# Performance work log

Hardware: AMD Instinct MI355X
Metric: run time of the kernel (lower is better)

The kernel has to match this reference:

```python
import jax, jax.numpy as jnp
import numpy as np

B = 128           # graphs per batch (cell.num_graphs)
N0 = 706          # genes per graph
NF = 3            # num_feature
DIM = 64          # dim_cell
LAYERS = 3        # layer_cell
VIEW_E = [2268, 6872, 3088, 3150]   # per-graph edges per view (from forward slices)
EPS = 1e-5


def _make_clusters():
    ns = [N0]
    cs = []
    for _ in range(LAYERS):
        c = np.arange(ns[-1]) // 2
        cs.append(c)
        ns.append(int(c.max()) + 1)
    return cs, ns

CLUSTERS, NS = _make_clusters()      # NS = [706, 353, 177, 89]
FINAL = NS[-1]                        # final_node


def _pool_edges(e, c):
    # PyG max_pool pool_edge: relabel by cluster, drop self-loops, coalesce
    s, d = c[e[0]], c[e[1]]
    m = s != d
    return np.unique(np.stack([s[m], d[m]]), axis=1)


def _with_self_loops(e, n):
    sl = np.arange(n, dtype=e.dtype)
    return np.concatenate([e, np.stack([sl, sl])], axis=1)


def _batch(e, n):
    off = (np.arange(B, dtype=e.dtype) * n)
    return (e[:, None, :] + off[None, :, None]).reshape(2, -1)


def setup_inputs():
    rng = np.random.default_rng(0)
    key = jax.random.key(0)
    ks = jax.random.split(key, 32)
    inp = {}
    for j, ne in enumerate(VIEW_E):
        src = rng.integers(0, N0, ne)
        dst = (src + 1 + rng.integers(0, N0 - 1, ne)) % N0
        raw = np.stack([src, dst]).astype(np.int64)
        for i in range(LAYERS):
            gat_e = _batch(_with_self_loops(raw, NS[i]), NS[i])
            inp[f"edges_v{j}_l{i}"] = jnp.asarray(gat_e, jnp.int32)
            raw = _pool_edges(raw, CLUSTERS[i])
    for i in range(LAYERS):
        cb = (CLUSTERS[i][None, :] + (np.arange(B) * NS[i + 1])[:, None]).reshape(-1)
        inp[f"cluster_l{i}"] = jnp.asarray(cb, jnp.int32)

    def nrm(k, shape, scale):
        return jax.random.normal(k, shape, jnp.float32) * scale

    inp["x"] = nrm(ks[0], (B * N0, NF), 1.0)
    dims = [NF, DIM, DIM]
    t = 1
    for i in range(LAYERS):
        inp[f"W{i}"] = nrm(ks[t], (dims[i], DIM), dims[i] ** -0.5); t += 1
        inp[f"asrc{i}"] = nrm(ks[t], (DIM,), 0.1); t += 1
        inp[f"adst{i}"] = nrm(ks[t], (DIM,), 0.1); t += 1
        inp[f"b{i}"] = jnp.zeros((DIM,), jnp.float32)
    inp["w_attn"] = nrm(ks[t], (DIM,), DIM ** -0.5); t += 1
    inp["w_lin0"] = nrm(ks[t], (4 * DIM, 4), (4 * DIM) ** -0.5); t += 1
    inp["b_lin0"] = jnp.zeros((4,), jnp.float32)
    inp["w_link0"] = nrm(ks[t], (DIM, DIM), DIM ** -0.5); t += 1
    inp["w_linkl"] = nrm(ks[t], (DIM, DIM), DIM ** -0.5); t += 1
    inp["w_link_"] = nrm(ks[t], (DIM, DIM), DIM ** -0.5); t += 1
    return inp


def _gat(x, e, W, a_s, a_d, b, n):
    # PyG GATConv, heads=1: h = xW; alpha_e = leaky_relu(a_s.h[src] + a_d.h[dst]);
    # softmax over edges per target; out = sum_e alpha * h[src] + bias
    h = x @ W
    src, dst = e[0], e[1]
    logits = jax.nn.leaky_relu(jnp.take(h @ a_s, src) + jnp.take(h @ a_d, dst), 0.2)
    m = jax.ops.segment_max(logits, dst, num_segments=n)
    p = jnp.exp(logits - jnp.take(m, dst))
    z = jax.ops.segment_sum(p, dst, num_segments=n)
    attn = p / jnp.take(z, dst)
    out = jax.ops.segment_sum(jnp.take(h, src, axis=0) * attn[:, None], dst, num_segments=n)
    return out + b


def _bn(x):
    # BatchNorm1d(affine=False), training-mode batch stats
    mu = x.mean(0)
    v = x.var(0)
    return (x - mu) * jax.lax.rsqrt(v + EPS)


def _forward(x, edges, clusters, gat_ps, w_attn, w_lin0, b_lin0, w_link0, w_linkl, w_link_):
    n_in = [B * NS[i] for i in range(LAYERS)]
    n_out = [B * NS[i + 1] for i in range(LAYERS)]
    views = []
    for j in range(4):
        h = x
        for i in range(LAYERS):
            W, a_s, a_d, bi = gat_ps[i]
            h = jax.nn.relu(_gat(h, edges[j][i], W, a_s, a_d, bi, n_in[i]))
            h = jax.ops.segment_max(h, clusters[i], num_segments=n_out[i])  # max_pool
            h = _bn(h)
        views.append(h)
    ALL = jnp.stack(views)                           # [4, M, DIM]
    Bm = jnp.einsum('vmd,d->mv', ALL, w_attn)        # linear_attn per view
    Bm = Bm / jnp.linalg.norm(Bm, axis=0, keepdims=True)
    A = jax.nn.softmax(jax.nn.leaky_relu(Bm.T @ Bm, 0.1), axis=-1)  # [4,4]
    ALLf = jnp.einsum('kmd,kl->lmd', ALL, A)         # bmm fusion
    Mn = ALLf.shape[1]
    E = ALLf.reshape(Mn, -1)                          # torch.reshape(ALL, (l,-1))
    E = E @ w_lin0 + b_lin0                           # linear_0
    w = jax.nn.softmax(E.mean(0))                     # [4]
    r = jnp.einsum('v,vmd->md', w, ALLf)
    r = jax.nn.selu(r @ w_link0)
    r = jax.nn.selu(r @ w_linkl)
    r = r @ w_link_
    return r.reshape(-1, FINAL * DIM)


def reference(x,
              edges_v0_l0, edges_v0_l1, edges_v0_l2,
              edges_v1_l0, edges_v1_l1, edges_v1_l2,
              edges_v2_l0, edges_v2_l1, edges_v2_l2,
              edges_v3_l0, edges_v3_l1, edges_v3_l2,
              cluster_l0, cluster_l1, cluster_l2,
              W0, asrc0, adst0, b0,
              W1, asrc1, adst1, b1,
              W2, asrc2, adst2, b2,
              w_attn, w_lin0, b_lin0, w_link0, w_linkl, w_link_):
    edges = [[edges_v0_l0, edges_v0_l1, edges_v0_l2],
             [edges_v1_l0, edges_v1_l1, edges_v1_l2],
             [edges_v2_l0, edges_v2_l1, edges_v2_l2],
             [edges_v3_l0, edges_v3_l1, edges_v3_l2]]
    clusters = [cluster_l0, cluster_l1, cluster_l2]
    gat_ps = [(W0, asrc0, adst0, b0), (W1, asrc1, adst1, b1), (W2, asrc2, adst2, b2)]
    return _forward(x, edges, clusters, gat_ps, w_attn, w_lin0, b_lin0,
                    w_link0, w_linkl, w_link_)
```

## Files before the change

### kernel.cpp

```cpp
#include <hip/hip_runtime.h>
#include <hip/hip_fp16.h>
#include <math.h>

#define DIM 64
#define M_FINAL (128*89)

static inline int cdiv(int a, int b) { return (a + b - 1) / b; }

typedef _Float16 v8h __attribute__((ext_vector_type(8)));
typedef _Float16 v4h __attribute__((ext_vector_type(4)));
typedef float v4f __attribute__((ext_vector_type(4)));

__device__ inline float rdlane(float v, int l) {
    return __int_as_float(__builtin_amdgcn_readlane(__float_as_int(v), l));
}
__device__ inline unsigned packpw(float p, unsigned src) {
    return ((unsigned)__half_as_ushort(__float2half(p)) << 16) | src;
}
__device__ inline float unpackpw(unsigned ep) {
    return __half2float(__ushort_as_half((unsigned short)(ep >> 16)));
}
__device__ inline __half2 u2h2(unsigned u) {
    union { unsigned u; __half2 h; } c; c.u = u; return c.h;
}

struct EdgeSets {
    const int* src[12];
    const int* dst[12];
    int ne[12];
};

struct L0Args {
    const float* x;
    __half* out[4];
    const int* rowptr[4];
    const int* colsrc[4];
    int ne[4];
    int nemax;
    double* dstats;
    const float* W;
    const float* as;
    const float* ad;
    const float* bias;
};

struct AggArgs {
    const __half* hp[4];
    void* out[4];
    const int* rowptr[4];
    const int* colsrc[4];
    int ne[4];
    int nemax;
    const float* sS;
    const float* sD;
    const float* bias;
    double* dstats;
};


__global__ void zero_kernel(float* __restrict__ p, int n) {
    int i = blockIdx.x * blockDim.x + threadIdx.x;
    if (i < n) p[i] = 0.f;
}

__global__ __launch_bounds__(768)
void csr_build_kernel(EdgeSets ES, int* __restrict__ rowptr_all,
                      int* __restrict__ colsrc_all) {
    __shared__ int cnt[768];
    __shared__ int cur[768];
    const int s = blockIdx.x;
    const int lay = s % 3;
    const int n = (lay == 0) ? 706 : (lay == 1) ? 353 : 177;
    const int ne = ES.ne[s];
    const int* __restrict__ src = ES.src[s];
    const int* __restrict__ dst = ES.dst[s];
    int* __restrict__ rowptr = rowptr_all + s * 768;
    int* __restrict__ colsrc = colsrc_all + s * 8192;
    const int t = threadIdx.x;

    cnt[t] = 0;
    __syncthreads();
    for (int k = t; k < ne; k += 768) atomicAdd(&cnt[dst[k]], 1);
    __syncthreads();
    int v = cnt[t];
    for (int off = 1; off < 768; off <<= 1) {
        int add = (t >= off) ? cnt[t - off] : 0;
        __syncthreads();
        cnt[t] += add;
        __syncthreads();
    }
    int excl = cnt[t] - v;
    if (t < n) { rowptr[t] = excl; cur[t] = excl; }
    if (t == n - 1) rowptr[n] = cnt[t];
    __syncthreads();
    for (int k = t; k < ne; k += 768) {
        int pos = atomicAdd(&cur[dst[k]], 1);
        colsrc[pos] = src[k];
    }
}

__global__ __launch_bounds__(512, 8)
void layer0_kernel(L0Args A) {
    constexpr int NPIN = 706, NPOUT = 353, HALF = 177;

    extern __shared__ char smem[];
    float* sredF = (float*)smem;
    float* fp = (float*)(smem + 4096);
    float* sSrc = fp; fp += NPIN;
    float* sDst = fp; fp += NPIN;
    float* hL4  = fp; fp += NPIN * 4;
    float* agg4 = fp; fp += 356 * 4;
    float* waL0 = fp; fp += 8;
    unsigned short* rp16 = (unsigned short*)fp;

    const int split = blockIdx.x >> 9;
    const int jg = blockIdx.x & 511;
    const int j = jg >> 7;
    const int g = jg & 127;
    const int tid = threadIdx.x;
    const int wave = tid >> 6;
    const int lane = tid & 63;

    const int n0c = split * HALF;
    const int n1c = min(NPOUT, n0c + HALF);
    const int ch0 = 2 * n0c;
    const int ch1 = 2 * n1c;

    const int* __restrict__ rowptr = A.rowptr[j];
    const int* __restrict__ colsrc = A.colsrc[j];
    const float* __restrict__ W = A.W;

    for (int k = tid; k <= NPIN; k += 512) rp16[k] = (unsigned short)rowptr[k];
    if (tid < 6) {
        int f = (tid < 3) ? tid : tid - 3;
        const float* av = (tid < 3) ? A.as : A.ad;
        float acc = 0.f;
        for (int d = 0; d < 64; ++d) acc += W[f * 64 + d] * av[d];
        waL0[tid] = acc;
    }
    __syncthreads();

    {
        const float* hb = A.x + (size_t)g * (NPIN * 3);
        for (int r = tid; r < NPIN; r += 512) {
            float h0 = hb[r * 3], h1 = hb[r * 3 + 1], h2 = hb[r * 3 + 2];
            hL4[r * 4] = h0; hL4[r * 4 + 1] = h1; hL4[r * 4 + 2] = h2; hL4[r * 4 + 3] = 0.f;
            sSrc[r] = h0 * waL0[0] + h1 * waL0[1] + h2 * waL0[2];
            sDst[r] = h0 * waL0[3] + h1 * waL0[4] + h2 * waL0[5];
        }
    }
    __syncthreads();

    const int child = ch0 + tid;
    if (child < ch1) {
        int s0 = rp16[child], e0 = rp16[child + 1];
        float sd = sDst[child];
        float m = -1e30f;
        for (int k = s0; k < e0; ++k) {
            float v = sSrc[colsrc[k]] + sd;
            v = (v >= 0.f) ? v : 0.2f * v;
            m = fmaxf(m, v);
        }
        float z = 0.f, a0 = 0.f, a1 = 0.f, a2 = 0.f;
        for (int k = s0; k < e0; ++k) {
            int sl = colsrc[k];
            float v = sSrc[sl] + sd;
            v = (v >= 0.f) ? v : 0.2f * v;
            float p = __expf(v - m);
            z += p;
            a0 += p * hL4[sl * 4];
            a1 += p * hL4[sl * 4 + 1];
            a2 += p * hL4[sl * 4 + 2];
        }
        float iz = 1.f / z;
        agg4[tid * 4]     = a0 * iz;
        agg4[tid * 4 + 1] = a1 * iz;
        agg4[tid * 4 + 2] = a2 * iz;
        agg4[tid * 4 + 3] = 0.f;
    }
    __syncthreads();

    const float w0 = W[lane], w1 = W[64 + lane], w2 = W[128 + lane];
    const float b_l = A.bias[lane];
    __half* outj = A.out[j];
    const float4* agg4v = (const float4*)agg4;
    float bs = 0.f, bs2 = 0.f;

    for (int c = n0c + wave; c < n1c; c += 8) {
        int lc = 2 * (c - n0c);
        float4 va = agg4v[lc];
        float4 vb = agg4v[lc + 1];
        float oa = va.x * w0 + va.y * w1 + va.z * w2 + b_l;
        float ob = vb.x * w0 + vb.y * w1 + vb.z * w2 + b_l;
        float vmax = fmaxf(fmaxf(oa, ob), 0.f);
        outj[((size_t)g * NPOUT + c) * 64 + lane] = __float2half(vmax);
        bs += vmax;
        bs2 += vmax * vmax;
    }
    sredF[wave * 64 + lane] = bs;
    sredF[512 + wave * 64 + lane] = bs2;
    __syncthreads();
    if (wave == 0) {
        float t1 = 0.f, t2 = 0.f;
        #pragma unroll
        for (int w = 0; w < 8; ++w) {
            t1 += sredF[w * 64 + lane];
            t2 += sredF[512 + w * 64 + lane];
        }
        atomicAdd(A.dstats + j * 128 + lane, (double)t1);
        atomicAdd(A.dstats + j * 128 + 64 + lane, (double)t2);
    }
}

__global__ void bn_finalize_kernel(const double* __restrict__ dstats,
                                   float* __restrict__ musig, int n_rows,
                                   const float* __restrict__ Wn,
                                   float* __restrict__ Wp, float* __restrict__ csh) {
    __shared__ float mur[128];
    int jv = blockIdx.x;
    int d = threadIdx.x;
    double mu = dstats[jv * 128 + d] / n_rows;
    double var = dstats[jv * 128 + 64 + d] / n_rows - mu * mu;
    float rs = rsqrtf((float)var + 1e-5f);
    musig[jv * 128 + d] = (float)mu;
    musig[jv * 128 + 64 + d] = rs;
    if (Wn != nullptr) {
        mur[d] = (float)mu; mur[64 + d] = rs;
        __syncthreads();
        float c = 0.f;
        for (int f = 0; f < 64; ++f) {
            float wp = mur[64 + f] * Wn[f * 64 + d];
            Wp[jv * 4096 + f * 64 + d] = wp;
            c += mur[f] * wp;
        }
        csh[jv * 64 + d] = c;
    }
}

__global__ __launch_bounds__(256, 4)
void proj_kernel(__half* __restrict__ buf, const float* __restrict__ Wp_all,
                 const float* __restrict__ csh_all,
                 const float* __restrict__ a_s, const float* __restrict__ a_d,
                 float* __restrict__ sS, float* __restrict__ sD, int npin) {
    __shared__ _Float16 Wt[64 * 64];
    const int j = blockIdx.y;
    const int tid = threadIdx.x;
    const int lane = tid & 63, wave = tid >> 6;
    const int lc = lane & 15, quad = lane >> 4;
    const int R = 128 * npin;
    __half* h = buf + (size_t)j * R * 64;
    const float* Wp = Wp_all + j * 4096;

    for (int k = tid; k < 4096; k += 256) {
        int f = k >> 6, d = k & 63;
        Wt[d * 64 + f] = (_Float16)Wp[k];
    }
    __syncthreads();

    v8h bfrag[4][2];
    #pragma unroll
    for (int t = 0; t < 4; ++t)
        #pragma unroll
        for (int s = 0; s < 2; ++s)
            bfrag[t][s] = *(const v8h*)&Wt[(t * 16 + lc) * 64 + s * 32 + quad * 8];

    float cshv[4], asv[4], adv[4];
    #pragma unroll
    for (int t = 0; t < 4; ++t) {
        cshv[t] = csh_all[j * 64 + t * 16 + lc];
        asv[t] = a_s[t * 16 + lc];
        adv[t] = a_d[t * 16 + lc];
    }

    const int ntiles = R >> 4;
    for (int tile = blockIdx.x * 4 + wave; tile < ntiles; tile += gridDim.x * 4) {
        const int rowbase = tile * 16;
        const __half* arow = h + ((size_t)(rowbase + lc)) * 64 + quad * 8;
        v8h a0 = *(const v8h*)arow;
        v8h a1 = *(const v8h*)(arow + 32);
        v4f acc[4];
        #pragma unroll
        for (int t = 0; t < 4; ++t) {
            acc[t] = (v4f){0.f, 0.f, 0.f, 0.f};
            acc[t] = __builtin_amdgcn_mfma_f32_16x16x32_f16(a0, bfrag[t][0], acc[t], 0, 0, 0);
            acc[t] = __builtin_amdgcn_mfma_f32_16x16x32_f16(a1, bfrag[t][1], acc[t], 0, 0, 0);
        }
        float pS[4] = {0.f, 0.f, 0.f, 0.f};
        float pD[4] = {0.f, 0.f, 0.f, 0.f};
        #pragma unroll
        for (int t = 0; t < 4; ++t) {
            #pragma unroll
            for (int r = 0; r < 4; ++r) {
                float o = acc[t][r] - cshv[t];
                h[((size_t)(rowbase + quad * 4 + r)) * 64 + t * 16 + lc] = __float2half(o);
                pS[r] += o * asv[t];
                pD[r] += o * adv[t];
            }
        }
        #pragma unroll
        for (int m = 1; m < 16; m <<= 1) {
            #pragma unroll
            for (int r = 0; r < 4; ++r) {
                pS[r] += __shfl_xor(pS[r], m, 64);
                pD[r] += __shfl_xor(pD[r], m, 64);
            }
        }
        if (lc == 0) {
            #pragma unroll
            for (int r = 0; r < 4; ++r) {
                sS[j * R + rowbase + quad * 4 + r] = pS[r];
                sD[j * R + rowbase + quad * 4 + r] = pD[r];
            }
        }
    }
}

template<int NPIN, typename OutT>
__global__ __launch_bounds__(512, 8)
void agg_kernel(AggArgs A) {
    constexpr int NPOUT = (NPIN + 1) / 2;
    constexpr int HALF = (NPOUT + 1) / 2;

    extern __shared__ char smem[];
    float* sredF = (float*)smem;
    float* fp = (float*)(smem + 4096);
    float* sSrc = fp; fp += NPIN;
    float* sDst = fp; fp += NPIN;
    unsigned* ep32 = (unsigned*)fp;
    unsigned short* rp16 = (unsigned short*)(ep32 + A.nemax);

    const int split = blockIdx.x >> 9;
    const int jg = blockIdx.x & 511;
    const int j = jg >> 7;
    const int g = jg & 127;
    const int tid = threadIdx.x;
    const int wave = tid >> 6;
    const int lane = tid & 63;
    const int qg = lane >> 4;
    const int lc = lane & 15;

    const int n0c = split * HALF;
    const int n1c = min(NPOUT, n0c + HALF);
    const int ch0 = 2 * n0c;
    const int ch1 = min(NPIN, 2 * n1c);

    const int* __restrict__ rowptr = A.rowptr[j];
    const int* __restrict__ colsrc = A.colsrc[j];
    const int ne = A.ne[j];
    const int sbase = (j * 128 + g) * NPIN;
    const __half* __restrict__ hpb = A.hp[j] + (size_t)g * NPIN * 64 + 4 * lc;

    for (int k = tid; k <= NPIN; k += 512) rp16[k] = (unsigned short)rowptr[k];
    for (int k = tid; k < ne; k += 512) ep32[k] = (unsigned)colsrc[k];
    for (int r = tid; r < NPIN; r += 512) {
        sSrc[r] = A.sS[sbase + r];
        sDst[r] = A.sD[sbase + r];
    }
    __syncthreads();

    for (int r = ch0 + tid; r < ch1; r += 512) {
        int s0 = rp16[r], e0 = rp16[r + 1];
        float sd = sDst[r];
        float m = -1e30f, z = 0.f;
        for (int k = s0; k < e0; ++k) {
            float v = sSrc[ep32[k] & 0xFFFFu] + sd;
            v = (v >= 0.f) ? v : 0.2f * v;
            if (v > m) { z = z * __expf(m - v) + 1.f; m = v; }
            else z += __expf(v - m);
        }
        float invz = 1.f / z;
        for (int k = s0; k < e0; ++k) {
            unsigned sl = ep32[k] & 0xFFFFu;
            float v = sSrc[sl] + sd;
            v = (v >= 0.f) ? v : 0.2f * v;
            ep32[k] = packpw(__expf(v - m) * invz, sl);
        }
    }
    __syncthreads();

    const float4 b4 = *(const float4*)(A.bias + 4 * lc);
    OutT* outj = (OutT*)A.out[j];
    float bs[4] = {0.f, 0.f, 0.f, 0.f};
    float bs2[4] = {0.f, 0.f, 0.f, 0.f};

    for (int c = n0c + wave; c < n1c; c += 8) {
        float vch[2][4];
        #pragma unroll
        for (int ch = 0; ch < 2; ++ch) {
            __half2 aA0 = u2h2(0), aA1 = u2h2(0);
            __half2 aB0 = u2h2(0), aB1 = u2h2(0);
            int child = 2 * c + ch;
            if (child < NPIN) {
                int s0 = rp16[child], e0 = rp16[child + 1];
                int k = s0;
                for (; k + 8 <= e0; k += 8) {
                    unsigned e0p = ep32[k + qg];
                    unsigned e1p = ep32[k + 4 + qg];
                    uint2 u0 = *(const uint2*)(hpb + (size_t)(e0p & 0xFFFFu) * 64);
                    uint2 u1 = *(const uint2*)(hpb + (size_t)(e1p & 0xFFFFu) * 64);
                    __half2 p0 = u2h2((e0p & 0xFFFF0000u) | (e0p >> 16));
                    __half2 p1 = u2h2((e1p & 0xFFFF0000u) | (e1p >> 16));
                    aA0 = __hfma2(u2h2(u0.x), p0, aA0);
                    aA1 = __hfma2(u2h2(u0.y), p0, aA1);
                    aB0 = __hfma2(u2h2(u1.x), p1, aB0);
                    aB1 = __hfma2(u2h2(u1.y), p1, aB1);
                }
                for (; k < e0; k += 4) {
                    int idx = k + qg;
                    unsigned ep = ep32[(idx < e0) ? idx : (e0 - 1)];
                    uint2 u0 = *(const uint2*)(hpb + (size_t)(ep & 0xFFFFu) * 64);
                    unsigned pb = (idx < e0) ? ((ep & 0xFFFF0000u) | (ep >> 16)) : 0u;
                    __half2 p0 = u2h2(pb);
                    aA0 = __hfma2(u2h2(u0.x), p0, aA0);
                    aA1 = __hfma2(u2h2(u0.y), p0, aA1);
                }
            }
            float2 f0 = __half22float2(aA0), f1 = __half22float2(aA1);
            float2 g0 = __half22float2(aB0), g1 = __half22float2(aB1);
            vch[ch][0] = f0.x + g0.x;
            vch[ch][1] = f0.y + g0.y;
            vch[ch][2] = f1.x + g1.x;
            vch[ch][3] = f1.y + g1.y;
        }
        #pragma unroll
        for (int m = 16; m < 64; m <<= 1) {
            #pragma unroll
            for (int r = 0; r < 4; ++r) {
                vch[0][r] += __shfl_xor(vch[0][r], m, 64);
                vch[1][r] += __shfl_xor(vch[1][r], m, 64);
            }
        }
        float vm[4];
        #pragma unroll
        for (int r = 0; r < 4; ++r) {
            float oa = vch[0][r] + ((const float*)&b4)[r];
            float ob = vch[1][r] + ((const float*)&b4)[r];
            vm[r] = fmaxf(fmaxf(oa, ob), 0.f);
            bs[r] += vm[r];
            bs2[r] += vm[r] * vm[r];
        }
        if (qg == 0) {
            if constexpr (sizeof(OutT) == 2) {
                v4h hv;
                #pragma unroll
                for (int r = 0; r < 4; ++r) hv[r] = (_Float16)vm[r];
                *(v4h*)((__half*)outj + ((size_t)g * NPOUT + c) * 64 + 4 * lc) = hv;
            } else {
                float4 fv = {vm[0], vm[1], vm[2], vm[3]};
                *(float4*)((float*)outj + ((size_t)g * NPOUT + c) * 64 + 4 * lc) = fv;
            }
        }
    }
    if (qg == 0) {
        #pragma unroll
        for (int r = 0; r < 4; ++r) {
            sredF[wave * 64 + 4 * lc + r] = bs[r];
            sredF[512 + wave * 64 + 4 * lc + r] = bs2[r];
        }
    }
    __syncthreads();
    if (wave == 0) {
        float t1 = 0.f, t2 = 0.f;
        #pragma unroll
        for (int w = 0; w < 8; ++w) {
            t1 += sredF[w * 64 + lane];
            t2 += sredF[512 + w * 64 + lane];
        }
        atomicAdd(A.dstats + j * 128 + lane, (double)t1);
        atomicAdd(A.dstats + j * 128 + 64 + lane, (double)t2);
    }
}

__global__ __launch_bounds__(256)
void head_reduce_kernel(const float* __restrict__ ALL, const float* __restrict__ musig,
                        const float* __restrict__ w_attn,
                        float* __restrict__ S, float* __restrict__ cm) {
    __shared__ float S_loc[16];
    __shared__ float cm_loc[256];
    const int t = threadIdx.x, wave = t >> 6, lane = t & 63;
    if (t < 16) S_loc[t] = 0.f;
    cm_loc[t] = 0.f;
    __syncthreads();
    const float wa = w_attn[lane];
    float cacc[4] = {0.f, 0.f, 0.f, 0.f};
    for (int m = blockIdx.x * 4 + wave; m < M_FINAL; m += gridDim.x * 4) {
        float b4[4];
        float csum = 0.f;
        #pragma unroll
        for (int v = 0; v < 4; ++v) {
            float val = (ALL[((size_t)v * M_FINAL + m) * 64 + lane] - musig[v * 128 + lane])
                        * musig[v * 128 + 64 + lane];
            csum += val;
            float p = val * wa;
            for (int off = 32; off > 0; off >>= 1) p += __shfl_down(p, off, 64);
            b4[v] = __shfl(p, 0, 64);
        }
        cacc[m & 3] += csum;
        if (lane < 16) atomicAdd(&S_loc[lane], b4[lane >> 2] * b4[lane & 3]);
    }
    #pragma unroll
    for (int q = 0; q < 4; ++q) atomicAdd(&cm_loc[q * 64 + lane], cacc[q]);
    __syncthreads();
    if (t < 16) atomicAdd(&S[t], S_loc[t]);
    atomicAdd(&cm[t], cm_loc[t]);
}

__global__ void fuse_small_kernel(const float* __restrict__ S, const float* __restrict__ cm,
                                  const float* __restrict__ w_lin0, const float* __restrict__ b_lin0,
                                  float* __restrict__ cvec) {
    const int lane = threadIdx.x;
    float pa0 = 0.f, pa1 = 0.f, pa2 = 0.f, pa3 = 0.f;
    #pragma unroll
    for (int q = 0; q < 4; ++q) {
        int c = q * 64 + lane;
        float cmv = cm[c] / (float)M_FINAL;
        pa0 += cmv * w_lin0[c * 4 + 0];
        pa1 += cmv * w_lin0[c * 4 + 1];
        pa2 += cmv * w_lin0[c * 4 + 2];
        pa3 += cmv * w_lin0[c * 4 + 3];
    }
    for (int off = 32; off > 0; off >>= 1) {
        pa0 += __shfl_down(pa0, off, 64);
        pa1 += __shfl_down(pa1, off, 64);
        pa2 += __shfl_down(pa2, off, 64);
        pa3 += __shfl_down(pa3, off, 64);
    }
    if (lane != 0) return;
    float e4[4] = {pa0 + b_lin0[0], pa1 + b_lin0[1], pa2 + b_lin0[2], pa3 + b_lin0[3]};
    float cn[4];
    for (int v = 0; v < 4; ++v) cn[v] = sqrtf(S[v * 4 + v]);
    float A[16];
    for (int u = 0; u < 4; ++u) {
        float row[4]; float mx = -1e30f;
        for (int v = 0; v < 4; ++v) {
            float g = S[u * 4 + v] / (cn[u] * cn[v]);
            g = (g >= 0.f) ? g : 0.1f * g;
            row[v] = g; mx = fmaxf(mx, g);
        }
        float sum = 0.f;
        for (int v = 0; v < 4; ++v) { row[v] = expf(row[v] - mx); sum += row[v]; }
        for (int v = 0; v < 4; ++v) A[u * 4 + v] = row[v] / sum;
    }
    float mx = fmaxf(fmaxf(e4[0], e4[1]), fmaxf(e4[2], e4[3]));
    float sum = 0.f, w[4];
    for (int v = 0; v < 4; ++v) { w[v] = expf(e4[v] - mx); sum += w[v]; }
    for (int v = 0; v < 4; ++v) w[v] /= sum;
    for (int k = 0; k < 4; ++k) {
        float c = 0.f;
        for (int v = 0; v < 4; ++v) c += A[k * 4 + v] * w[v];
        cvec[k] = c;
    }
}

__global__ __launch_bounds__(256)
void head_out_kernel(const float* __restrict__ ALL, const float* __restrict__ musig,
                     const float* __restrict__ cvec,
                     const float* __restrict__ W0, const float* __restrict__ W1,
                     const float* __restrict__ W2, float* __restrict__ outp) {
    __shared__ float Wl[3][64 * 64];
    const int t = threadIdx.x, wave = t >> 6, lane = t & 63;
    for (int k = t; k < 4096; k += 256) {
        Wl[0][k] = W0[k]; Wl[1][k] = W1[k]; Wl[2][k] = W2[k];
    }
    __syncthreads();
    const float c0 = cvec[0], c1 = cvec[1], c2 = cvec[2], c3 = cvec[3];
    const float scale = 1.0507009873554805f;
    const float alpha = 1.6732632423543772f;
    for (int m = blockIdx.x * 4 + wave; m < M_FINAL; m += gridDim.x * 4) {
        float r =
            c0 * ((ALL[((size_t)0 * M_FINAL + m) * 64 + lane] - musig[0 * 128 + lane]) * musig[0 * 128 + 64 + lane]) +
            c1 * ((ALL[((size_t)1 * M_FINAL + m) * 64 + lane] - musig[1 * 128 + lane]) * musig[1 * 128 + 64 + lane]) +
            c2 * ((ALL[((size_t)2 * M_FINAL + m) * 64 + lane] - musig[2 * 128 + lane]) * musig[2 * 128 + 64 + lane]) +
            c3 * ((ALL[((size_t)3 * M_FINAL + m) * 64 + lane] - musig[3 * 128 + lane]) * musig[3 * 128 + 64 + lane]);
        #pragma unroll
        for (int s = 0; s < 3; ++s) {
            float o0 = 0.f, o1 = 0.f, o2 = 0.f, o3 = 0.f;
            #pragma unroll
            for (int f = 0; f < 64; f += 4) {
                o0 += rdlane(r, f)     * Wl[s][f * 64 + lane];
                o1 += rdlane(r, f + 1) * Wl[s][(f + 1) * 64 + lane];
                o2 += rdlane(r, f + 2) * Wl[s][(f + 2) * 64 + lane];
                o3 += rdlane(r, f + 3) * Wl[s][(f + 3) * 64 + lane];
            }
            float o = (o0 + o1) + (o2 + o3);
            if (s < 2) o = (o > 0.f) ? scale * o : scale * alpha * expm1f(o);
            r = o;
        }
        outp[(size_t)m * 64 + lane] = r;
    }
}

extern "C" void kernel_launch(void* const* d_in, const int* in_sizes, int n_in,
                              void* d_out, int out_size, void* d_ws, size_t ws_size,
                              hipStream_t stream) {
    const float* x = (const float*)d_in[15];

    float* ws = (float*)d_ws;
    double* dstats_all = (double*)ws;
    float*  cm         = ws + 3072;
    float*  S          = ws + 3328;
    float*  cvec       = ws + 3344;
    float*  musig_all  = ws + 3584;
    float*  Wp_all     = ws + 5120;
    float*  csh_all    = ws + 37888;
    int*    rowptr_all = (int*)(ws + 38400);
    int*    colsrc_all = (int*)(ws + 47616);
    float*  sS1        = ws + 145920;
    float*  sD1        = sS1 + 180736;
    float*  sS2        = sD1 + 180736;
    float*  sD2        = sS2 + 90624;
    __half* A16        = (__half*)(sD2 + 90624);
    __half* B16        = (__half*)((float*)A16 + 5783552);
    float*  ALLb       = (float*)B16 + 2899968;
    const size_t as0h = (size_t)128 * 353 * 64;
    const size_t as1h = (size_t)128 * 177 * 64;

    EdgeSets ES;
    int nemax[3] = {0, 0, 0};
    for (int s = 0; s < 12; ++s) {
        const int* e = (const int*)d_in[s];
        int E = in_sizes[s] / 2;
        ES.src[s] = e;
        ES.dst[s] = e + E;
        ES.ne[s] = E / 128;
        int lay = s % 3;
        if (ES.ne[s] > nemax[lay]) nemax[lay] = ES.ne[s];
    }

    int SM0 = 4096 + (706 * 6 + 356 * 4 + 8) * 4 + 708 * 2;
    SM0 = (SM0 + 15) & ~15;
    int SMa1 = 4096 + (2 * 353) * 4 + nemax[1] * 4 + 355 * 2;
    SMa1 = (SMa1 + 15) & ~15;
    int SMa2 = 4096 + (2 * 177) * 4 + nemax[2] * 4 + 179 * 2;
    SMa2 = (SMa2 + 15) & ~15;
    (void)hipFuncSetAttribute(reinterpret_cast<const void*>(&layer0_kernel),
                              hipFuncAttributeMaxDynamicSharedMemorySize, SM0);
    (void)hipFuncSetAttribute(reinterpret_cast<const void*>(&agg_kernel<353, __half>),
                              hipFuncAttributeMaxDynamicSharedMemorySize, SMa1);
    (void)hipFuncSetAttribute(reinterpret_cast<const void*>(&agg_kernel<177, float>),
                              hipFuncAttributeMaxDynamicSharedMemorySize, SMa2);

    zero_kernel<<<cdiv(3584, 256), 256, 0, stream>>>(ws, 3584);
    csr_build_kernel<<<12, 768, 0, stream>>>(ES, rowptr_all, colsrc_all);

    {
        L0Args A;
        A.x = x;
        for (int j = 0; j < 4; ++j) {
            int s = j * 3;
            A.rowptr[j] = rowptr_all + s * 768;
            A.colsrc[j] = colsrc_all + s * 8192;
            A.ne[j] = ES.ne[s];
            A.out[j] = A16 + j * as0h;
        }
        A.nemax = nemax[0];
        A.dstats = dstats_all;
        A.W = (const float*)d_in[16];
        A.as = (const float*)d_in[17];
        A.ad = (const float*)d_in[18];
        A.bias = (const float*)d_in[19];
        layer0_kernel<<<1024, 512, SM0, stream>>>(A);
    }
    bn_finalize_kernel<<<4, 64, 0, stream>>>(dstats_all, musig_all, 128 * 353,
                                             (const float*)d_in[20], Wp_all, csh_all);

    proj_kernel<<<dim3(256, 4), 256, 0, stream>>>(A16, Wp_all, csh_all,
                                                  (const float*)d_in[21], (const float*)d_in[22],
                                                  sS1, sD1, 353);
    {
        AggArgs A;
        for (int j = 0; j < 4; ++j) {
            int s = j * 3 + 1;
            A.rowptr[j] = rowptr_all + s * 768;
            A.colsrc[j] = colsrc_all + s * 8192;
            A.ne[j] = ES.ne[s];
            A.hp[j] = A16 + j * as0h;
            A.out[j] = B16 + j * as1h;
        }
        A.nemax = nemax[1];
        A.sS = sS1; A.sD = sD1;
        A.bias = (const float*)d_in[23];
        A.dstats = dstats_all + 512;
        agg_kernel<353, __half><<<1024, 512, SMa1, stream>>>(A);
    }
    bn_finalize_kernel<<<4, 64, 0, stream>>>(dstats_all + 512, musig_all + 512, 128 * 177,
                                             (const float*)d_in[24], Wp_all + 16384, csh_all + 256);

    proj_kernel<<<dim3(256, 4), 256, 0, stream>>>(B16, Wp_all + 16384, csh_all + 256,
                                                  (const float*)d_in[25], (const float*)d_in[26],
                                                  sS2, sD2, 177);
    {
        AggArgs A;
        for (int j = 0; j < 4; ++j) {
            int s = j * 3 + 2;
            A.rowptr[j] = rowptr_all + s * 768;
            A.colsrc[j] = colsrc_all + s * 8192;
            A.ne[j] = ES.ne[s];
            A.hp[j] = B16 + j * as1h;
            A.out[j] = ALLb + (size_t)j * M_FINAL * 64;
        }
        A.nemax = nemax[2];
        A.sS = sS2; A.sD = sD2;
        A.bias = (const float*)d_in[27];
        A.dstats = dstats_all + 1024;
        agg_kernel<177, float><<<1024, 512, SMa2, stream>>>(A);
    }
    bn_finalize_kernel<<<4, 64, 0, stream>>>(dstats_all + 1024, musig_all + 1024, 128 * 89,
                                             nullptr, nullptr, nullptr);

    const float* musig2 = musig_all + 1024;
    head_reduce_kernel<<<256, 256, 0, stream>>>(ALLb, musig2, (const float*)d_in[28], S, cm);
    fuse_small_kernel<<<1, 64, 0, stream>>>(S, cm, (const float*)d_in[29], (const float*)d_in[30], cvec);
    head_out_kernel<<<256, 256, 0, stream>>>(ALLb, musig2, cvec,
                                             (const float*)d_in[31], (const float*)d_in[32],
                                             (const float*)d_in[33], (float*)d_out);
}
```

Before: 335.3 us.

## Split pooled GAT aggregation into quarters and load only the local edge range

The layer-1 and layer-2 aggregation kernels now split each (view, graph) pair's pooled output nodes into four chunks instead of two, doubling the grid to 2048 blocks. Each block loads only the slice of edge sources its child rows need, offset by the row pointer at the chunk start, rather than the whole edge list. The gather loop also gets a 16-edge unrolled body so more independent loads are in flight. The costs are duplicated per-block setup (row pointers and node scores are still loaded in full) and more blocks for the partial statistics reduction.

```diff
diff --git a/kernel.cpp b/kernel.cpp
--- a/kernel.cpp
+++ b/kernel.cpp
@@ -319,7 +319,7 @@
 __global__ __launch_bounds__(512, 8)
 void agg_kernel(AggArgs A) {
     constexpr int NPOUT = (NPIN + 1) / 2;
-    constexpr int HALF = (NPOUT + 1) / 2;
+    constexpr int QTR = (NPOUT + 3) / 4;
 
     extern __shared__ char smem[];
     float* sredF = (float*)smem;
@@ -339,19 +339,21 @@
     const int qg = lane >> 4;
     const int lc = lane & 15;
 
-    const int n0c = split * HALF;
-    const int n1c = min(NPOUT, n0c + HALF);
+    const int n0c = split * QTR;
+    const int n1c = min(NPOUT, n0c + QTR);
     const int ch0 = 2 * n0c;
     const int ch1 = min(NPIN, 2 * n1c);
 
     const int* __restrict__ rowptr = A.rowptr[j];
     const int* __restrict__ colsrc = A.colsrc[j];
-    const int ne = A.ne[j];
     const int sbase = (j * 128 + g) * NPIN;
     const __half* __restrict__ hpb = A.hp[j] + (size_t)g * NPIN * 64 + 4 * lc;
 
+    const int es0 = rowptr[ch0];
+    const int es1 = rowptr[ch1];
+
     for (int k = tid; k <= NPIN; k += 512) rp16[k] = (unsigned short)rowptr[k];
-    for (int k = tid; k < ne; k += 512) ep32[k] = (unsigned)colsrc[k];
+    for (int k = es0 + tid; k < es1; k += 512) ep32[k - es0] = (unsigned)colsrc[k];
     for (int r = tid; r < NPIN; r += 512) {
         sSrc[r] = A.sS[sbase + r];
         sDst[r] = A.sD[sbase + r];
@@ -359,7 +361,7 @@
     __syncthreads();
 
     for (int r = ch0 + tid; r < ch1; r += 512) {
-        int s0 = rp16[r], e0 = rp16[r + 1];
+        int s0 = rp16[r] - es0, e0 = rp16[r + 1] - es0;
         float sd = sDst[r];
         float m = -1e30f, z = 0.f;
         for (int k = s0; k < e0; ++k) {
@@ -391,8 +393,30 @@
             __half2 aB0 = u2h2(0), aB1 = u2h2(0);
             int child = 2 * c + ch;
             if (child < NPIN) {
-                int s0 = rp16[child], e0 = rp16[child + 1];
+                int s0 = rp16[child] - es0, e0 = rp16[child + 1] - es0;
                 int k = s0;
+                for (; k + 16 <= e0; k += 16) {
+                    unsigned ea = ep32[k + qg];
+                    unsigned eb = ep32[k + 4 + qg];
+                    unsigned ec = ep32[k + 8 + qg];
+                    unsigned ed = ep32[k + 12 + qg];
+                    uint2 u0 = *(const uint2*)(hpb + (size_t)(ea & 0xFFFFu) * 64);
+                    uint2 u1 = *(const uint2*)(hpb + (size_t)(eb & 0xFFFFu) * 64);
+                    uint2 u2 = *(const uint2*)(hpb + (size_t)(ec & 0xFFFFu) * 64);
+                    uint2 u3 = *(const uint2*)(hpb + (size_t)(ed & 0xFFFFu) * 64);
+                    __half2 p0 = u2h2((ea & 0xFFFF0000u) | (ea >> 16));
+                    __half2 p1 = u2h2((eb & 0xFFFF0000u) | (eb >> 16));
+                    __half2 p2 = u2h2((ec & 0xFFFF0000u) | (ec >> 16));
+                    __half2 p3 = u2h2((ed & 0xFFFF0000u) | (ed >> 16));
+                    aA0 = __hfma2(u2h2(u0.x), p0, aA0);
+                    aA1 = __hfma2(u2h2(u0.y), p0, aA1);
+                    aB0 = __hfma2(u2h2(u1.x), p1, aB0);
+                    aB1 = __hfma2(u2h2(u1.y), p1, aB1);
+                    aA0 = __hfma2(u2h2(u2.x), p2, aA0);
+                    aA1 = __hfma2(u2h2(u2.y), p2, aA1);
+                    aB0 = __hfma2(u2h2(u3.x), p3, aB0);
+                    aB1 = __hfma2(u2h2(u3.y), p3, aB1);
+                }
                 for (; k + 8 <= e0; k += 8) {
                     unsigned e0p = ep32[k + qg];
                     unsigned e1p = ep32[k + 4 + qg];
@@ -681,7 +705,7 @@
         A.sS = sS1; A.sD = sD1;
         A.bias = (const float*)d_in[23];
         A.dstats = dstats_all + 512;
-        agg_kernel<353, __half><<<1024, 512, SMa1, stream>>>(A);
+        agg_kernel<353, __half><<<2048, 512, SMa1, stream>>>(A);
     }
     bn_finalize_kernel<<<4, 64, 0, stream>>>(dstats_all + 512, musig_all + 512, 128 * 177,
                                              (const float*)d_in[24], Wp_all + 16384, csh_all + 256);
@@ -703,7 +727,7 @@
         A.sS = sS2; A.sD = sD2;
         A.bias = (const float*)d_in[27];
         A.dstats = dstats_all + 1024;
-        agg_kernel<177, float><<<1024, 512, SMa2, stream>>>(A);
+        agg_kernel<177, float><<<2048, 512, SMa2, stream>>>(A);
     }
     bn_finalize_kernel<<<4, 64, 0, stream>>>(dstats_all + 1024, musig_all + 1024, 128 * 89,
                                              nullptr, nullptr, nullptr);
```

New measurement: 349.6 us. 4.3% more time.
